# Kernel tuning notes

Hardware: AMD Instinct MI355X
Metric: run time of the kernel (lower is better)

Reference implementation:

```python
import jax, jax.numpy as jnp
import numpy as np

QLEN, MLEN, CMLEN, BSZ, D_MODEL = 1024, 1024, 512, 2, 1024
N_HEAD, D_HEAD, D_INNER = 16, 64, 4096
KLEN = MLEN + CMLEN + QLEN
LN_EPS = 1e-5


def _layer_norm(x, scale, bias):
    mu = jnp.mean(x, axis=-1, keepdims=True)
    var = jnp.var(x, axis=-1, keepdims=True)
    return (x - mu) * jax.lax.rsqrt(var + LN_EPS) * scale + bias


def _rel_shift(x):
    # x: [qlen, klen, bsz, n_head]  (Transformer-XL relative shift)
    q, k, b, n = x.shape
    x = jnp.concatenate([jnp.zeros((q, 1, b, n), x.dtype), x], axis=1)
    x = x.reshape(k + 1, q, b, n)[1:]
    return x.reshape(q, k, b, n)


def setup_inputs() -> dict:
    key = jax.random.key(0)
    ks = jax.random.split(key, 10)
    s = 0.02
    # causal mask: query i (absolute pos MLEN_TOT+i) cannot attend to key j > MLEN_TOT+i
    mlen_tot = KLEN - QLEN
    i = jnp.arange(QLEN)[:, None]
    j = jnp.arange(KLEN)[None, :]
    attn_mask = j > (i + mlen_tot)
    return {
        "input_ids": jax.random.normal(ks[0], (QLEN, BSZ, D_MODEL), jnp.float32),
        "pos_emb": jax.random.normal(ks[1], (KLEN, D_MODEL), jnp.float32),
        "mem": jax.random.normal(ks[2], (MLEN, BSZ, D_MODEL), jnp.float32),
        "c_mem": jax.random.normal(ks[3], (CMLEN, BSZ, D_MODEL), jnp.float32),
        "attn_mask": attn_mask,
        "qkv_w": jax.random.normal(ks[4], (D_MODEL, 3 * N_HEAD * D_HEAD), jnp.float32) * s,
        "r_w": jax.random.normal(ks[5], (D_MODEL, N_HEAD * D_HEAD), jnp.float32) * s,
        "o_w": jax.random.normal(ks[6], (N_HEAD * D_HEAD, D_MODEL), jnp.float32) * s,
        "r_w_bias": jax.random.normal(ks[7], (N_HEAD, D_HEAD), jnp.float32) * s,
        "r_r_bias": jax.random.normal(ks[8], (N_HEAD, D_HEAD), jnp.float32) * s,
        "ln_attn_scale": jnp.ones((D_MODEL,), jnp.float32),
        "ln_attn_bias": jnp.zeros((D_MODEL,), jnp.float32),
        "ff_w1": jax.random.normal(ks[9], (D_MODEL, D_INNER), jnp.float32) * s,
        "ff_b1": jnp.zeros((D_INNER,), jnp.float32),
        "ff_w2": jax.random.normal(jax.random.fold_in(key, 11), (D_INNER, D_MODEL), jnp.float32) * s,
        "ff_b2": jnp.zeros((D_MODEL,), jnp.float32),
        "ln_ff_scale": jnp.ones((D_MODEL,), jnp.float32),
        "ln_ff_bias": jnp.zeros((D_MODEL,), jnp.float32),
    }


def reference(input_ids, pos_emb, mem, c_mem, attn_mask, qkv_w, r_w, o_w,
              r_w_bias, r_r_bias, ln_attn_scale, ln_attn_bias,
              ff_w1, ff_b1, ff_w2, ff_b2, ln_ff_scale, ln_ff_bias):
    qlen, bsz, d_model = input_ids.shape
    n_head, d_head = r_w_bias.shape
    scale = 1.0 / np.sqrt(d_head)

    # _concat_memories + cat with current sequence (seq-first, dim 0)
    mems = jnp.concatenate([mem, c_mem], axis=0)
    cat = jnp.concatenate([mems, input_ids], axis=0)          # [klen, b, d]

    w_heads = cat @ qkv_w                                     # [klen, b, 3*h*dh]
    w_q, w_k, w_v = jnp.split(w_heads, 3, axis=-1)
    w_q = w_q[-qlen:]
    klen = w_k.shape[0]

    w_q = w_q.reshape(qlen, bsz, n_head, d_head)
    w_k = w_k.reshape(klen, bsz, n_head, d_head)
    w_v = w_v.reshape(klen, bsz, n_head, d_head)
    r_k = (pos_emb @ r_w).reshape(klen, n_head, d_head)       # [klen, h, dh]

    AC = jnp.einsum('ibnd,jbnd->ijbn', w_q + r_w_bias, w_k)
    BD = jnp.einsum('ibnd,jnd->ijbn', w_q + r_r_bias, r_k)
    BD = _rel_shift(BD)
    attn_score = (AC + BD) * scale                            # [q, k, b, h]

    attn_score = jnp.where(attn_mask[:, :, None, None], jnp.float32(-1e30), attn_score)
    attn_prob = jax.nn.softmax(attn_score, axis=1)

    attn_vec = jnp.einsum('ijbn,jbnd->ibnd', attn_prob, w_v)
    attn_vec = attn_vec.reshape(qlen, bsz, n_head * d_head)
    attn_out = attn_vec @ o_w

    # post-lnorm residual (pre_lnorm=False)
    attn_res = _layer_norm(input_ids + attn_out, ln_attn_scale, ln_attn_bias)

    # PositionwiseFF (post-lnorm)
    h = jax.nn.relu(attn_res @ ff_w1 + ff_b1) @ ff_w2 + ff_b2
    out = _layer_norm(attn_res + h, ln_ff_scale, ln_ff_bias)
    return out
```

## Files before the change

kernel.cpp:

```cpp
#include <hip/hip_runtime.h>
#include <hip/hip_bf16.h>

#define QLEN 1024
#define KLEN 2560
#define MTOT 1536
#define BSZ 2
#define NH 16
#define DH 64
#define DMODEL 1024
#define DINNER 4096

typedef short bf16x8 __attribute__((ext_vector_type(8)));
typedef float f32x4  __attribute__((ext_vector_type(4)));

__device__ __forceinline__ short f2bf(float f) {
    union { float f; unsigned u; } v; v.f = f;
    unsigned r = v.u + 0x7FFFu + ((v.u >> 16) & 1u);
    return (short)(r >> 16);
}
__device__ __forceinline__ float bf2f(short s) {
    union { unsigned u; float f; } v; v.u = ((unsigned)(unsigned short)s) << 16;
    return v.f;
}
__device__ __forceinline__ unsigned pack2(float a, float b) {
    unsigned pk;
    asm("v_cvt_pk_bf16_f32 %0, %1, %2" : "=v"(pk) : "v"(a), "v"(b));
    return pk;
}

#define GLOAD16(g, l)                                                        \
    __builtin_amdgcn_global_load_lds(                                        \
        (const __attribute__((address_space(1))) unsigned int*)(g),          \
        (__attribute__((address_space(3))) unsigned int*)(l), 16, 0, 0)

__device__ __forceinline__ void tr_body(
    const float* __restrict__ in, short* __restrict__ out,
    int K, int N, int bx, int by, int tid, float (*ts)[65])
{
    const int k0 = by * 64, n0 = bx * 64;
    const int r = tid >> 2, cb = (tid & 3) * 16;
    #pragma unroll
    for (int u = 0; u < 16; u += 4) {
        const float4 v = *(const float4*)(in + (size_t)(k0 + r) * N + n0 + cb + u);
        ts[r][cb + u] = v.x; ts[r][cb + u + 1] = v.y;
        ts[r][cb + u + 2] = v.z; ts[r][cb + u + 3] = v.w;
    }
    __syncthreads();
    #pragma unroll
    for (int p = 0; p < 4; p++) {
        const int wr_ = (tid >> 4) + p * 16;
        const int c   = (tid & 15) * 4;
        uint2 pk;
        pk.x = pack2(ts[c][wr_], ts[c + 1][wr_]);
        pk.y = pack2(ts[c + 2][wr_], ts[c + 3][wr_]);
        *(uint2*)(out + (size_t)(n0 + wr_) * K + k0 + c) = pk;
    }
}

__global__ __launch_bounds__(256) void prep_all(
    const float* __restrict__ mem, const float* __restrict__ cmem,
    const float* __restrict__ inp, short* __restrict__ catb,
    const float* __restrict__ pos, short* __restrict__ posb,
    const float* __restrict__ qkv_w, short* __restrict__ qkv_wt,
    const float* __restrict__ r_w, short* __restrict__ r_wt,
    const float* __restrict__ o_w, short* __restrict__ o_wt,
    const float* __restrict__ ff_w1, short* __restrict__ ff1t,
    const float* __restrict__ ff_w2, short* __restrict__ ff2t)
{
    __shared__ float ts[64][65];
    const int bid = blockIdx.x;
    const int tid = threadIdx.x;
    if (bid < 2560) {
        const int i = bid * 256 + tid;
        const int row = i >> 7, c = (i & 127) * 8;
        const float* src;
        if (row < 2048)      src = mem  + (size_t)row * 1024;
        else if (row < 3072) src = cmem + (size_t)(row - 2048) * 1024;
        else                 src = inp  + (size_t)(row - 3072) * 1024;
        const float4 a = *(const float4*)(src + c);
        const float4 b = *(const float4*)(src + c + 4);
        uint4 o;
        o.x = pack2(a.x, a.y); o.y = pack2(a.z, a.w);
        o.z = pack2(b.x, b.y); o.w = pack2(b.z, b.w);
        *(uint4*)(catb + (size_t)i * 8) = o;
    } else if (bid < 3840) {
        const int i = (bid - 2560) * 256 + tid;
        const float4 a = *(const float4*)(pos + (size_t)i * 8);
        const float4 b = *(const float4*)(pos + (size_t)i * 8 + 4);
        uint4 o;
        o.x = pack2(a.x, a.y); o.y = pack2(a.z, a.w);
        o.z = pack2(b.x, b.y); o.w = pack2(b.z, b.w);
        *(uint4*)(posb + (size_t)i * 8) = o;
    } else if (bid < 4608) {
        const int r = bid - 3840; tr_body(qkv_w, qkv_wt, 1024, 3072, r % 48, r / 48, tid, ts);
    } else if (bid < 4864) {
        const int r = bid - 4608; tr_body(r_w, r_wt, 1024, 1024, r % 16, r / 16, tid, ts);
    } else if (bid < 5120) {
        const int r = bid - 4864; tr_body(o_w, o_wt, 1024, 1024, r % 16, r / 16, tid, ts);
    } else if (bid < 6144) {
        const int r = bid - 5120; tr_body(ff_w1, ff1t, 1024, 4096, r % 64, r / 64, tid, ts);
    } else {
        const int r = bid - 6144; tr_body(ff_w2, ff2t, 4096, 1024, r % 16, r / 16, tid, ts);
    }
}

__global__ __launch_bounds__(256) void vt_conv(
    const short* __restrict__ wh, short* __restrict__ vt)
{
    __shared__ short Ts[64][72];
    const int j0 = blockIdx.x * 64;
    const int bn = blockIdx.y;
    const int b = bn >> 4, n = bn & 15;
    const int tid = threadIdx.x;
    {
        const int key = tid >> 2, c = (tid & 3) * 16;
        const short* p = wh + ((size_t)(j0 + key) * BSZ + b) * 3072 + 2048 + n * 64 + c;
        *(bf16x8*)&Ts[key][c]     = *(const bf16x8*)p;
        *(bf16x8*)&Ts[key][c + 8] = *(const bf16x8*)(p + 8);
    }
    __syncthreads();
    {
        const int d = tid >> 2, kc = (tid & 3) * 16;
        __attribute__((aligned(16))) short tmp[16];
        #pragma unroll
        for (int u = 0; u < 16; u++) tmp[u] = Ts[kc + u][d];
        short* q = vt + ((size_t)(bn * 64) + d) * KLEN + j0 + kc;
        *(uint4*)q       = *(uint4*)tmp;
        *(uint4*)(q + 8) = *((uint4*)tmp + 1);
    }
}

__device__ __forceinline__ void gemm_core(
    const short* __restrict__ A, const short* __restrict__ Bt,
    short* As, short* Bs, int Kfull, int klen, int bm, int bn,
    int tid, f32x4 acc[4][4])
{
    const int w  = tid >> 6;
    const int l  = tid & 63;
    const int lg = l >> 4, lc = l & 15;
    const int wr = w >> 1, wc = w & 1;
    const int srow = 2 * w * 16 + (l >> 2);
    const int scol = (l & 3) * 8;
    const size_t aoff0 = (size_t)(bm + srow) * Kfull + scol;
    const size_t boff0 = (size_t)(bn + srow) * Kfull + scol;
    const size_t rstep = (size_t)16 * Kfull;
    short* lA0 = As + 2 * w * 512;
    short* lA1 = As + (2 * w + 1) * 512;
    short* lB0 = Bs + 2 * w * 512;
    short* lB1 = Bs + (2 * w + 1) * 512;

    for (int k0 = 0; k0 < klen; k0 += 32) {
        GLOAD16(A + aoff0 + k0, lA0);
        GLOAD16(A + aoff0 + rstep + k0, lA1);
        GLOAD16(Bt + boff0 + k0, lB0);
        GLOAD16(Bt + boff0 + rstep + k0, lB1);
        __syncthreads();
        bf16x8 af[4], bfr[4];
        #pragma unroll
        for (int m = 0; m < 4; m++)
            af[m] = *(const bf16x8*)(As + (wr * 64 + m * 16 + lc) * 32 + lg * 8);
        #pragma unroll
        for (int n = 0; n < 4; n++)
            bfr[n] = *(const bf16x8*)(Bs + (wc * 64 + n * 16 + lc) * 32 + lg * 8);
        #pragma unroll
        for (int m = 0; m < 4; m++)
            #pragma unroll
            for (int n = 0; n < 4; n++)
                acc[m][n] = __builtin_amdgcn_mfma_f32_16x16x32_bf16(
                    af[m], bfr[n], acc[m][n], 0, 0, 0);
        __syncthreads();
    }
}

__global__ __launch_bounds__(256) void gemm_g12(
    const short* __restrict__ catb, const short* __restrict__ qkv_wt,
    short* __restrict__ whb,
    const short* __restrict__ posb, const short* __restrict__ r_wt,
    short* __restrict__ rkb)
{
    __shared__ short As[4096], Bs[4096];
    const int tid = threadIdx.x;
    int id = blockIdx.x;
    const short *A, *Bt; short* Cb; int N, bm, bn;
    if (id < 384) {
        A = catb; Bt = qkv_wt; Cb = whb; N = 3072;
        bm = (id >> 4) * 128; bn = (8 + (id & 15)) * 128;
    } else if (id < 768) {
        id -= 384;
        A = catb; Bt = qkv_wt; Cb = whb; N = 3072;
        bm = (24 + id / 24) * 128; bn = (id % 24) * 128;
    } else {
        id -= 768;
        A = posb; Bt = r_wt; Cb = rkb; N = 1024;
        bm = (id / 8) * 128; bn = (id % 8) * 128;
    }

    f32x4 acc[4][4];
    #pragma unroll
    for (int m = 0; m < 4; m++)
        #pragma unroll
        for (int n = 0; n < 4; n++) acc[m][n] = (f32x4){0.f, 0.f, 0.f, 0.f};
    gemm_core(A, Bt, As, Bs, 1024, 1024, bm, bn, tid, acc);

    const int w = tid >> 6, l = tid & 63, lg = l >> 4, lc = l & 15;
    const int wr = w >> 1, wc = w & 1;
    #pragma unroll
    for (int m = 0; m < 4; m++)
        #pragma unroll
        for (int n = 0; n < 4; n++) {
            const int col = bn + wc * 64 + n * 16 + lc;
            #pragma unroll
            for (int r = 0; r < 4; r++) {
                const int row = bm + wr * 64 + m * 16 + lg * 4 + r;
                Cb[(size_t)row * N + col] = f2bf(acc[m][n][r]);
            }
        }
}

__global__ __launch_bounds__(256) void gemm_relu(
    const short* __restrict__ A, const short* __restrict__ Bt,
    const float* __restrict__ bias, short* __restrict__ Cb,
    int N, int K)
{
    __shared__ short As[4096], Bs[4096];
    const int tid = threadIdx.x;
    const int bm = blockIdx.y * 128, bn = blockIdx.x * 128;
    f32x4 acc[4][4];
    #pragma unroll
    for (int m = 0; m < 4; m++)
        #pragma unroll
        for (int n = 0; n < 4; n++) acc[m][n] = (f32x4){0.f, 0.f, 0.f, 0.f};
    gemm_core(A, Bt, As, Bs, K, K, bm, bn, tid, acc);

    const int w = tid >> 6, l = tid & 63, lg = l >> 4, lc = l & 15;
    const int wr = w >> 1, wc = w & 1;
    #pragma unroll
    for (int m = 0; m < 4; m++)
        #pragma unroll
        for (int n = 0; n < 4; n++) {
            const int col = bn + wc * 64 + n * 16 + lc;
            const float bv = bias[col];
            #pragma unroll
            for (int r = 0; r < 4; r++) {
                const int row = bm + wr * 64 + m * 16 + lg * 4 + r;
                Cb[(size_t)row * N + col] = f2bf(fmaxf(acc[m][n][r] + bv, 0.0f));
            }
        }
}

__global__ __launch_bounds__(256) void gemm_split(
    const short* __restrict__ A, const short* __restrict__ Bt,
    float* __restrict__ C0, float* __restrict__ C1,
    int N, int Kfull, int Ksub)
{
    __shared__ short As[4096], Bs[4096];
    const int tid = threadIdx.x;
    const int z = blockIdx.z;
    const int bm = blockIdx.y * 128, bn = blockIdx.x * 128;
    float* C = z ? C1 : C0;
    f32x4 acc[4][4];
    #pragma unroll
    for (int m = 0; m < 4; m++)
        #pragma unroll
        for (int n = 0; n < 4; n++) acc[m][n] = (f32x4){0.f, 0.f, 0.f, 0.f};
    gemm_core(A + z * Ksub, Bt + z * Ksub, As, Bs, Kfull, Ksub, bm, bn, tid, acc);

    const int w = tid >> 6, l = tid & 63, lg = l >> 4, lc = l & 15;
    const int wr = w >> 1, wc = w & 1;
    #pragma unroll
    for (int m = 0; m < 4; m++)
        #pragma unroll
        for (int n = 0; n < 4; n++) {
            const int col = bn + wc * 64 + n * 16 + lc;
            #pragma unroll
            for (int r = 0; r < 4; r++) {
                const int row = bm + wr * 64 + m * 16 + lg * 4 + r;
                C[(size_t)row * N + col] = acc[m][n][r];
            }
        }
}

__global__ __launch_bounds__(512, 2) void attn_mfma(
    const short* __restrict__ wh,
    const short* __restrict__ vt,
    const short* __restrict__ rk,
    const float* __restrict__ rwb,
    const float* __restrict__ rrb,
    short* __restrict__ po,
    float* __restrict__ ml)
{
    __shared__ __align__(16) short Ks[64 * 64];
    __shared__ __align__(16) short Vs[64 * 64];
    __shared__ __align__(16) short Rs[256 * 64];
    __shared__ __align__(16) short Ps[8][16 * 64];

    const int bid = blockIdx.x;
    const int ibp = (bid >> 3) & 7;
    const int z   = (bid >> 6) & 1;
    const int bn  = ((bid & 7) << 2) | (bid >> 7);
    const int i0  = ibp * 128;
    const int b   = bn >> 4, n = bn & 15;
    const int tid = threadIdx.x;
    const int w   = tid >> 6;
    const int l   = tid & 63;
    const int lg  = l >> 4;
    const int lc  = l & 15;
    const int i_base = i0 + 16 * w;

    bf16x8 aqw[2], aqr[2];
    {
        const int i = i_base + lc;
        const short* qp = wh + ((size_t)(MTOT + i) * BSZ + b) * 3072 + n * 64;
        #pragma unroll
        for (int kc2 = 0; kc2 < 2; kc2++) {
            const bf16x8 q8 = *(const bf16x8*)(qp + kc2 * 32 + lg * 8);
            const int d0 = kc2 * 32 + lg * 8;
            #pragma unroll
            for (int e = 0; e < 8; e++) {
                const float qv = bf2f(q8[e]);
                aqw[kc2][e] = f2bf(qv + rwb[n * 64 + d0 + e]);
                aqr[kc2][e] = f2bf(qv + rrb[n * 64 + d0 + e]);
            }
        }
    }

    f32x4 o_acc[4];
    #pragma unroll
    for (int nt = 0; nt < 4; nt++) o_acc[nt] = (f32x4){0.f, 0.f, 0.f, 0.f};
    float mrun[4]  = {0.f, 0.f, 0.f, 0.f};
    float lpart[4] = {0.f, 0.f, 0.f, 0.f};

    const int jend   = i0 + 1664;
    const int jhalf  = i0 / 2 + 832;
    const int jstart = z ? jhalf : 0;
    const int jstop  = z ? jend  : jhalf;

    const int kr = tid >> 3, kc = tid & 7;
    const size_t whK = (size_t)b * 3072 + 1024 + n * 64;
    const size_t vtK = (size_t)(bn * 64) * KLEN;

    {
        const int mbase0 = jstart - i0 + 896;
        #pragma unroll
        for (int u = 0; u < 2; u++) {
            const int m = mbase0 + kr + 64 * u;
            bf16x8 rv = (bf16x8){0, 0, 0, 0, 0, 0, 0, 0};
            if (m < KLEN)
                rv = *(const bf16x8*)(rk + (size_t)m * 1024 + n * 64 + kc * 8);
            const int slot = m & 255;
            *(bf16x8*)(Rs + slot * 64 + ((kc ^ (slot & 7)) * 8)) = rv;
        }
    }
    bf16x8 pk, pv, pr;
    pk = *(const bf16x8*)(wh + (size_t)(jstart + kr) * (BSZ * 3072) + whK + kc * 8);
    pv = *(const bf16x8*)(vt + vtK + (size_t)kr * KLEN + jstart + kc * 8);
    {
        const int m = jstart - i0 + 1024 + kr;
        pr = (m < KLEN)
            ? *(const bf16x8*)(rk + (size_t)m * 1024 + n * 64 + kc * 8)
            : (bf16x8){0, 0, 0, 0, 0, 0, 0, 0};
    }

    for (int j0 = jstart; j0 < jstop; j0 += 64) {
        const int mbase = j0 - i0 + 896;
        __syncthreads();
        *(bf16x8*)(Ks + kr * 64 + ((kc ^ (kr & 7)) * 8)) = pk;
        *(bf16x8*)(Vs + kr * 64 + ((kc ^ (kr & 7)) * 8)) = pv;
        {
            const int slot = (mbase + 128 + kr) & 255;
            *(bf16x8*)(Rs + slot * 64 + ((kc ^ (slot & 7)) * 8)) = pr;
        }
        const int jn = j0 + 64;
        if (jn < jstop) {
            pk = *(const bf16x8*)(wh + (size_t)(jn + kr) * (BSZ * 3072) + whK + kc * 8);
            pv = *(const bf16x8*)(vt + vtK + (size_t)kr * KLEN + jn + kc * 8);
            const int m = jn - i0 + 1024 + kr;
            pr = (m < KLEN)
                ? *(const bf16x8*)(rk + (size_t)m * 1024 + n * 64 + kc * 8)
                : (bf16x8){0, 0, 0, 0, 0, 0, 0, 0};
        }
        __syncthreads();

        __builtin_amdgcn_s_setprio(1);
        f32x4 sfr[4];
        #pragma unroll
        for (int jt = 0; jt < 4; jt++) {
            const int row = 16 * jt + lc;
            const int c0 = (lg ^ (row & 7)) * 8, c1 = ((4 + lg) ^ (row & 7)) * 8;
            const bf16x8 bk0 = *(const bf16x8*)(Ks + row * 64 + c0);
            const bf16x8 bk1 = *(const bf16x8*)(Ks + row * 64 + c1);
            f32x4 acc = (f32x4){0.f, 0.f, 0.f, 0.f};
            acc = __builtin_amdgcn_mfma_f32_16x16x32_bf16(aqw[0], bk0, acc, 0, 0, 0);
            acc = __builtin_amdgcn_mfma_f32_16x16x32_bf16(aqw[1], bk1, acc, 0, 0, 0);
            sfr[jt] = acc;
        }
        f32x4 dr[5];
        #pragma unroll
        for (int mt = 0; mt < 5; mt++) {
            const int slot = (mbase + 16 * mt + lc + 112 - 16 * w) & 255;
            const int c0 = (lg ^ (slot & 7)) * 8, c1 = ((4 + lg) ^ (slot & 7)) * 8;
            const bf16x8 br0 = *(const bf16x8*)(Rs + slot * 64 + c0);
            const bf16x8 br1 = *(const bf16x8*)(Rs + slot * 64 + c1);
            f32x4 acc = (f32x4){0.f, 0.f, 0.f, 0.f};
            acc = __builtin_amdgcn_mfma_f32_16x16x32_bf16(aqr[0], br0, acc, 0, 0, 0);
            acc = __builtin_amdgcn_mfma_f32_16x16x32_bf16(aqr[1], br1, acc, 0, 0, 0);
            dr[mt] = acc;
        }
        __builtin_amdgcn_s_setprio(0);

        #pragma unroll
        for (int r = 0; r < 4; r++) {
            const int q   = 4 * lg + r;
            const int o   = lc + 15 - q;
            const int src = (l & 48) | (o & 15);
            float sv[4];
            float mx = -1e30f;
            #pragma unroll
            for (int jt = 0; jt < 4; jt++) {
                const float v0 = __shfl(dr[jt][r], src);
                const float v1 = __shfl(dr[jt + 1][r], src);
                const float bd = (o < 16) ? v0 : v1;
                float s = (sfr[jt][r] + bd) * 0.125f;
                if (z) {
                    const int j = j0 + 16 * jt + lc;
                    if (j > i_base + q + MTOT) s = -1e30f;
                }
                sv[jt] = s;
                mx = fmaxf(mx, s);
            }
            if (__any(mx - mrun[r] > 8.0f)) {
                #pragma unroll
                for (int msk = 1; msk <= 8; msk <<= 1)
                    mx = fmaxf(mx, __shfl_xor(mx, msk));
                const float mnew = fmaxf(mrun[r], mx);
                const float corr = __expf(mrun[r] - mnew);
                mrun[r] = mnew;
                lpart[r] *= corr;
                #pragma unroll
                for (int nt = 0; nt < 4; nt++) o_acc[nt][r] *= corr;
            }
            float p0 = __expf(sv[0] - mrun[r]);
            float p1 = __expf(sv[1] - mrun[r]);
            float p2 = __expf(sv[2] - mrun[r]);
            float p3 = __expf(sv[3] - mrun[r]);
            lpart[r] += (p0 + p1) + (p2 + p3);
            const unsigned pk01 = pack2(p0, p1);
            const unsigned pk23 = pack2(p2, p3);
            short* pw = Ps[w] + q * 64 + (lc & 7);
            const int qs = q & 7;
            pw[(((0 + (lc >> 3)) ^ qs) * 8)] = (short)(pk01 & 0xffffu);
            pw[(((2 + (lc >> 3)) ^ qs) * 8)] = (short)(pk01 >> 16);
            pw[(((4 + (lc >> 3)) ^ qs) * 8)] = (short)(pk23 & 0xffffu);
            pw[(((6 + (lc >> 3)) ^ qs) * 8)] = (short)(pk23 >> 16);
        }

        asm volatile("s_waitcnt lgkmcnt(0)" ::: "memory");
        __builtin_amdgcn_sched_barrier(0);

        __builtin_amdgcn_s_setprio(1);
        const int pc0 = (lg ^ (lc & 7)) * 8, pc1 = ((4 + lg) ^ (lc & 7)) * 8;
        const bf16x8 pa0 = *(const bf16x8*)(Ps[w] + lc * 64 + pc0);
        const bf16x8 pa1 = *(const bf16x8*)(Ps[w] + lc * 64 + pc1);
        #pragma unroll
        for (int nt = 0; nt < 4; nt++) {
            const int row = 16 * nt + lc;
            const int c0 = (lg ^ (row & 7)) * 8, c1 = ((4 + lg) ^ (row & 7)) * 8;
            const bf16x8 bv0 = *(const bf16x8*)(Vs + row * 64 + c0);
            const bf16x8 bv1 = *(const bf16x8*)(Vs + row * 64 + c1);
            o_acc[nt] = __builtin_amdgcn_mfma_f32_16x16x32_bf16(pa0, bv0, o_acc[nt], 0, 0, 0);
            o_acc[nt] = __builtin_amdgcn_mfma_f32_16x16x32_bf16(pa1, bv1, o_acc[nt], 0, 0, 0);
        }
        __builtin_amdgcn_s_setprio(0);
    }

    const size_t blk = (size_t)z * 256 + ibp * 32 + bn;
    #pragma unroll
    for (int r = 0; r < 4; r++) {
        float lr = lpart[r];
        #pragma unroll
        for (int msk = 1; msk <= 8; msk <<= 1)
            lr += __shfl_xor(lr, msk);
        const int q = 16 * w + 4 * lg + r;
        #pragma unroll
        for (int nt = 0; nt < 4; nt++)
            po[(blk * 128 + q) * 64 + 16 * nt + lc] = f2bf(o_acc[nt][r]);
        if (lc == 0) {
            ml[(blk * 128 + q) * 2 + 0] = mrun[r];
            ml[(blk * 128 + q) * 2 + 1] = lr;
        }
    }
}

__global__ __launch_bounds__(256) void attn_merge(
    const short* __restrict__ po, const float* __restrict__ ml,
    short* __restrict__ av)
{
    const int blk = blockIdx.x;
    const int ib2 = blk >> 5, bn = blk & 31;
    const int b = bn >> 4, n = bn & 15;
    const int tid = threadIdx.x;
    const int q64 = tid >> 2, dc = (tid & 3) * 16;
    const int i = ib2 * 64 + q64;
    const size_t r0 = ((size_t)(i >> 7) * 32 + bn) * 128 + (i & 127);
    const size_t r1 = ((size_t)(256 + (i >> 7) * 32 + bn)) * 128 + (i & 127);
    const float m0 = ml[r0 * 2], l0 = ml[r0 * 2 + 1];
    const float m1 = ml[r1 * 2], l1 = ml[r1 * 2 + 1];
    const float M = fmaxf(m0, m1);
    const float c0 = __expf(m0 - M), c1 = __expf(m1 - M);
    const float invL = 1.0f / (l0 * c0 + l1 * c1);
    const bf16x8 a0 = *(const bf16x8*)(po + r0 * 64 + dc);
    const bf16x8 a1 = *(const bf16x8*)(po + r0 * 64 + dc + 8);
    const bf16x8 b0 = *(const bf16x8*)(po + r1 * 64 + dc);
    const bf16x8 b1 = *(const bf16x8*)(po + r1 * 64 + dc + 8);
    __attribute__((aligned(16))) short ov[16];
    #pragma unroll
    for (int e = 0; e < 8; e++) {
        ov[e]     = f2bf((bf2f(a0[e]) * c0 + bf2f(b0[e]) * c1) * invL);
        ov[e + 8] = f2bf((bf2f(a1[e]) * c0 + bf2f(b1[e]) * c1) * invL);
    }
    short* op = av + ((size_t)i * BSZ + b) * 1024 + n * 64 + dc;
    *(uint4*)op       = *(uint4*)ov;
    *(uint4*)(op + 8) = *((uint4*)ov + 1);
}

template <bool WB, bool HASB>
__global__ __launch_bounds__(256) void ln_fuse(
    const float* __restrict__ p0, const float* __restrict__ p1,
    const float* __restrict__ badd, const float* __restrict__ res,
    const float* __restrict__ scale, const float* __restrict__ bias,
    float* __restrict__ out, short* __restrict__ outb)
{
    const int row = blockIdx.x;
    const int tid = threadIdx.x;
    const size_t base = (size_t)row * 1024 + tid * 4;
    const float4 a = *(const float4*)(p0 + base);
    const float4 b = *(const float4*)(p1 + base);
    const float4 rv = *(const float4*)(res + base);
    float v[4] = {a.x + b.x + rv.x, a.y + b.y + rv.y,
                  a.z + b.z + rv.z, a.w + b.w + rv.w};
    if (HASB) {
        const float4 bb = *(const float4*)(badd + tid * 4);
        v[0] += bb.x; v[1] += bb.y; v[2] += bb.z; v[3] += bb.w;
    }
    float s  = v[0] + v[1] + v[2] + v[3];
    float ss = v[0]*v[0] + v[1]*v[1] + v[2]*v[2] + v[3]*v[3];
    #pragma unroll
    for (int off = 32; off >= 1; off >>= 1) {
        s  += __shfl_down(s, off);
        ss += __shfl_down(ss, off);
    }
    __shared__ float red[8];
    const int lane = tid & 63, wid = tid >> 6;
    if (lane == 0) { red[wid] = s; red[4 + wid] = ss; }
    __syncthreads();
    if (tid == 0) {
        red[0] = red[0] + red[1] + red[2] + red[3];
        red[4] = red[4] + red[5] + red[6] + red[7];
    }
    __syncthreads();
    const float mean = red[0] * (1.0f / 1024.0f);
    const float var  = red[4] * (1.0f / 1024.0f) - mean * mean;
    const float rstd = rsqrtf(var + 1e-5f);
    const float4 sc = *(const float4*)(scale + tid * 4);
    const float4 bi = *(const float4*)(bias + tid * 4);
    float4 o;
    o.x = (v[0] - mean) * rstd * sc.x + bi.x;
    o.y = (v[1] - mean) * rstd * sc.y + bi.y;
    o.z = (v[2] - mean) * rstd * sc.z + bi.z;
    o.w = (v[3] - mean) * rstd * sc.w + bi.w;
    *(float4*)(out + base) = o;
    if (WB) {
        uint2 pk;
        pk.x = pack2(o.x, o.y);
        pk.y = pack2(o.z, o.w);
        *(uint2*)(outb + base) = pk;
    }
}

extern "C" void kernel_launch(void* const* d_in, const int* in_sizes, int n_in,
                              void* d_out, int out_size, void* d_ws, size_t ws_size,
                              hipStream_t stream) {
    const float* input_ids = (const float*)d_in[0];
    const float* pos_emb   = (const float*)d_in[1];
    const float* mem       = (const float*)d_in[2];
    const float* c_mem     = (const float*)d_in[3];
    const float* qkv_w     = (const float*)d_in[5];
    const float* r_w       = (const float*)d_in[6];
    const float* o_w       = (const float*)d_in[7];
    const float* r_w_bias  = (const float*)d_in[8];
    const float* r_r_bias  = (const float*)d_in[9];
    const float* ln_a_s    = (const float*)d_in[10];
    const float* ln_a_b    = (const float*)d_in[11];
    const float* ff_w1     = (const float*)d_in[12];
    const float* ff_b1     = (const float*)d_in[13];
    const float* ff_w2     = (const float*)d_in[14];
    const float* ff_b2     = (const float*)d_in[15];
    const float* ln_f_s    = (const float*)d_in[16];
    const float* ln_f_b    = (const float*)d_in[17];

    char* base = (char*)d_ws;
    short* o_wt   = (short*)(base + 0);
    short* ff1t   = (short*)(base + 2097152);
    short* ff2t   = (short*)(base + 10485760);
    short* whb    = (short*)(base + 18874368);
    short* rkb    = (short*)(base + 50331648);
    short* qkv_wt = (short*)(base + 55574528);
    short* catb   = (short*)(base + 61865984);
    short* posb   = (short*)(base + 72351744);
    short* r_wt   = (short*)(base + 77594624);
    short* vtb    = (short*)(base + 55574528);
    short* po     = (short*)(base + 66060288);
    float* mlb    = (float*)(base + 74448896);
    short* avb    = (short*)(base + 74973184);
    float* hp0    = (float*)(base + 18874368);
    float* hp1    = (float*)(base + 27262976);
    float* ares   = (float*)(base + 35651584);
    short* aresb  = (short*)(base + 44040192);
    short* h1b    = (short*)(base + 48234496);

    const dim3 thr(256);

    prep_all<<<dim3(7168), thr, 0, stream>>>(
        mem, c_mem, input_ids, catb, pos_emb, posb,
        qkv_w, qkv_wt, r_w, r_wt, o_w, o_wt, ff_w1, ff1t, ff_w2, ff2t);
    gemm_g12<<<dim3(928), thr, 0, stream>>>(catb, qkv_wt, whb, posb, r_wt, rkb);
    vt_conv<<<dim3(40, 32), thr, 0, stream>>>(whb, vtb);
    attn_mfma<<<dim3(512), dim3(512), 0, stream>>>(
        whb, vtb, rkb, r_w_bias, r_r_bias, po, mlb);
    attn_merge<<<dim3(512), thr, 0, stream>>>(po, mlb, avb);
    gemm_split<<<dim3(8, 16, 2), thr, 0, stream>>>(
        avb, o_wt, hp0, hp1, 1024, 1024, 512);
    ln_fuse<true, false><<<dim3(2048), thr, 0, stream>>>(
        hp0, hp1, nullptr, input_ids, ln_a_s, ln_a_b, ares, aresb);
    gemm_relu<<<dim3(32, 16), thr, 0, stream>>>(aresb, ff1t, ff_b1, h1b, 4096, 1024);
    gemm_split<<<dim3(8, 16, 2), thr, 0, stream>>>(
        h1b, ff2t, hp0, hp1, 1024, 4096, 2048);
    ln_fuse<false, true><<<dim3(2048), thr, 0, stream>>>(
        hp0, hp1, ff_b2, ares, ln_f_s, ln_f_b, (float*)d_out, nullptr);
}
```

Before: 274.3 us.

## Double-buffer K/V tiles in attention and XCD-swizzle GEMM block mapping

The attention kernel now keeps two LDS buffers for the K and V tiles and prefetches two tiles ahead. This lets it drop the second __syncthreads per iteration, and the R ring buffer is pre-filled one tile further ahead. Separately, all GEMM kernels switch to a 1D grid whose block index is swizzled across the 8 XCDs, so neighbouring tiles share an L2. The double buffering adds LDS use, which may limit occupancy at 2 blocks of 512 threads. The R-slot indexing across the 256-row ring must also stay correct, since one barrier was removed.

Result: no change. 273.9 us (-0.1%).

```diff
diff --git a/kernel.cpp b/kernel.cpp
--- a/kernel.cpp
+++ b/kernel.cpp
@@ -180,7 +180,8 @@
 {
     __shared__ short As[4096], Bs[4096];
     const int tid = threadIdx.x;
-    int id = blockIdx.x;
+    const int id0 = blockIdx.x;
+    int id = (id0 & 7) * 116 + (id0 >> 3);
     const short *A, *Bt; short* Cb; int N, bm, bn;
     if (id < 384) {
         A = catb; Bt = qkv_wt; Cb = whb; N = 3072;
@@ -224,7 +225,11 @@
 {
     __shared__ short As[4096], Bs[4096];
     const int tid = threadIdx.x;
-    const int bm = blockIdx.y * 128, bn = blockIdx.x * 128;
+    const int nbx = N >> 7;
+    const int lid = blockIdx.x;
+    const int nwg8 = gridDim.x >> 3;
+    const int swz = (lid & 7) * nwg8 + (lid >> 3);
+    const int bn = (swz % nbx) * 128, bm = (swz / nbx) * 128;
     f32x4 acc[4][4];
     #pragma unroll
     for (int m = 0; m < 4; m++)
@@ -255,8 +260,14 @@
 {
     __shared__ short As[4096], Bs[4096];
     const int tid = threadIdx.x;
-    const int z = blockIdx.z;
-    const int bm = blockIdx.y * 128, bn = blockIdx.x * 128;
+    const int nbx = N >> 7;
+    const int lid = blockIdx.x;
+    const int nwg8 = gridDim.x >> 3;
+    const int swz = (lid & 7) * nwg8 + (lid >> 3);
+    const int bn = (swz % nbx) * 128;
+    const int rest = swz / nbx;
+    const int bm = (rest & 15) * 128;
+    const int z = rest >> 4;
     float* C = z ? C1 : C0;
     f32x4 acc[4][4];
     #pragma unroll
@@ -289,8 +300,8 @@
     short* __restrict__ po,
     float* __restrict__ ml)
 {
-    __shared__ __align__(16) short Ks[64 * 64];
-    __shared__ __align__(16) short Vs[64 * 64];
+    __shared__ __align__(16) short Ks[2][64 * 64];
+    __shared__ __align__(16) short Vs[2][64 * 64];
     __shared__ __align__(16) short Rs[256 * 64];
     __shared__ __align__(16) short Ps[8][16 * 64];
 
@@ -338,48 +349,56 @@
     const int kr = tid >> 3, kc = tid & 7;
     const size_t whK = (size_t)b * 3072 + 1024 + n * 64;
     const size_t vtK = (size_t)(bn * 64) * KLEN;
-
+    const int mbase0 = jstart - i0 + 896;
+
+    #pragma unroll
+    for (int u = 0; u < 3; u++) {
+        const int m = mbase0 + kr + 64 * u;
+        bf16x8 rv = (bf16x8){0, 0, 0, 0, 0, 0, 0, 0};
+        if (m < KLEN)
+            rv = *(const bf16x8*)(rk + (size_t)m * 1024 + n * 64 + kc * 8);
+        const int slot = m & 255;
+        *(bf16x8*)(Rs + slot * 64 + ((kc ^ (slot & 7)) * 8)) = rv;
+    }
     {
-        const int mbase0 = jstart - i0 + 896;
-        #pragma unroll
-        for (int u = 0; u < 2; u++) {
-            const int m = mbase0 + kr + 64 * u;
-            bf16x8 rv = (bf16x8){0, 0, 0, 0, 0, 0, 0, 0};
-            if (m < KLEN)
-                rv = *(const bf16x8*)(rk + (size_t)m * 1024 + n * 64 + kc * 8);
-            const int slot = m & 255;
-            *(bf16x8*)(Rs + slot * 64 + ((kc ^ (slot & 7)) * 8)) = rv;
-        }
-    }
-    bf16x8 pk, pv, pr;
-    pk = *(const bf16x8*)(wh + (size_t)(jstart + kr) * (BSZ * 3072) + whK + kc * 8);
-    pv = *(const bf16x8*)(vt + vtK + (size_t)kr * KLEN + jstart + kc * 8);
+        const bf16x8 k0 = *(const bf16x8*)(wh + (size_t)(jstart + kr) * (BSZ * 3072) + whK + kc * 8);
+        const bf16x8 v0 = *(const bf16x8*)(vt + vtK + (size_t)kr * KLEN + jstart + kc * 8);
+        *(bf16x8*)(Ks[0] + kr * 64 + ((kc ^ (kr & 7)) * 8)) = k0;
+        *(bf16x8*)(Vs[0] + kr * 64 + ((kc ^ (kr & 7)) * 8)) = v0;
+    }
+    bf16x8 pk = (bf16x8){0,0,0,0,0,0,0,0}, pv = pk, pr;
     {
-        const int m = jstart - i0 + 1024 + kr;
-        pr = (m < KLEN)
-            ? *(const bf16x8*)(rk + (size_t)m * 1024 + n * 64 + kc * 8)
-            : (bf16x8){0, 0, 0, 0, 0, 0, 0, 0};
-    }
-
+        const int jn = jstart + 64;
+        if (jn < jstop) {
+            pk = *(const bf16x8*)(wh + (size_t)(jn + kr) * (BSZ * 3072) + whK + kc * 8);
+            pv = *(const bf16x8*)(vt + vtK + (size_t)kr * KLEN + jn + kc * 8);
+        }
+        const int m = mbase0 + 192 + kr;
+        pr = (m < KLEN) ? *(const bf16x8*)(rk + (size_t)m * 1024 + n * 64 + kc * 8)
+                        : (bf16x8){0, 0, 0, 0, 0, 0, 0, 0};
+    }
+
+    int cur = 0;
     for (int j0 = jstart; j0 < jstop; j0 += 64) {
         const int mbase = j0 - i0 + 896;
         __syncthreads();
-        *(bf16x8*)(Ks + kr * 64 + ((kc ^ (kr & 7)) * 8)) = pk;
-        *(bf16x8*)(Vs + kr * 64 + ((kc ^ (kr & 7)) * 8)) = pv;
+        *(bf16x8*)(Ks[cur ^ 1] + kr * 64 + ((kc ^ (kr & 7)) * 8)) = pk;
+        *(bf16x8*)(Vs[cur ^ 1] + kr * 64 + ((kc ^ (kr & 7)) * 8)) = pv;
         {
-            const int slot = (mbase + 128 + kr) & 255;
+            const int mw = mbase + 192 + kr;
+            const int slot = mw & 255;
             *(bf16x8*)(Rs + slot * 64 + ((kc ^ (slot & 7)) * 8)) = pr;
         }
-        const int jn = j0 + 64;
-        if (jn < jstop) {
-            pk = *(const bf16x8*)(wh + (size_t)(jn + kr) * (BSZ * 3072) + whK + kc * 8);
-            pv = *(const bf16x8*)(vt + vtK + (size_t)kr * KLEN + jn + kc * 8);
-            const int m = jn - i0 + 1024 + kr;
-            pr = (m < KLEN)
-                ? *(const bf16x8*)(rk + (size_t)m * 1024 + n * 64 + kc * 8)
-                : (bf16x8){0, 0, 0, 0, 0, 0, 0, 0};
-        }
-        __syncthreads();
+        {
+            const int jn = j0 + 128;
+            if (jn < jstop) {
+                pk = *(const bf16x8*)(wh + (size_t)(jn + kr) * (BSZ * 3072) + whK + kc * 8);
+                pv = *(const bf16x8*)(vt + vtK + (size_t)kr * KLEN + jn + kc * 8);
+            }
+            const int m = mbase + 256 + kr;
+            pr = (m < KLEN) ? *(const bf16x8*)(rk + (size_t)m * 1024 + n * 64 + kc * 8)
+                            : (bf16x8){0, 0, 0, 0, 0, 0, 0, 0};
+        }
 
         __builtin_amdgcn_s_setprio(1);
         f32x4 sfr[4];
@@ -387,8 +406,8 @@
         for (int jt = 0; jt < 4; jt++) {
             const int row = 16 * jt + lc;
             const int c0 = (lg ^ (row & 7)) * 8, c1 = ((4 + lg) ^ (row & 7)) * 8;
-            const bf16x8 bk0 = *(const bf16x8*)(Ks + row * 64 + c0);
-            const bf16x8 bk1 = *(const bf16x8*)(Ks + row * 64 + c1);
+            const bf16x8 bk0 = *(const bf16x8*)(Ks[cur] + row * 64 + c0);
+            const bf16x8 bk1 = *(const bf16x8*)(Ks[cur] + row * 64 + c1);
             f32x4 acc = (f32x4){0.f, 0.f, 0.f, 0.f};
             acc = __builtin_amdgcn_mfma_f32_16x16x32_bf16(aqw[0], bk0, acc, 0, 0, 0);
             acc = __builtin_amdgcn_mfma_f32_16x16x32_bf16(aqw[1], bk1, acc, 0, 0, 0);
@@ -465,12 +484,13 @@
         for (int nt = 0; nt < 4; nt++) {
             const int row = 16 * nt + lc;
             const int c0 = (lg ^ (row & 7)) * 8, c1 = ((4 + lg) ^ (row & 7)) * 8;
-            const bf16x8 bv0 = *(const bf16x8*)(Vs + row * 64 + c0);
-            const bf16x8 bv1 = *(const bf16x8*)(Vs + row * 64 + c1);
+            const bf16x8 bv0 = *(const bf16x8*)(Vs[cur] + row * 64 + c0);
+            const bf16x8 bv1 = *(const bf16x8*)(Vs[cur] + row * 64 + c1);
             o_acc[nt] = __builtin_amdgcn_mfma_f32_16x16x32_bf16(pa0, bv0, o_acc[nt], 0, 0, 0);
             o_acc[nt] = __builtin_amdgcn_mfma_f32_16x16x32_bf16(pa1, bv1, o_acc[nt], 0, 0, 0);
         }
         __builtin_amdgcn_s_setprio(0);
+        cur ^= 1;
     }
 
     const size_t blk = (size_t)z * 256 + ibp * 32 + bn;
@@ -628,12 +648,12 @@
     attn_mfma<<<dim3(512), dim3(512), 0, stream>>>(
         whb, vtb, rkb, r_w_bias, r_r_bias, po, mlb);
     attn_merge<<<dim3(512), thr, 0, stream>>>(po, mlb, avb);
-    gemm_split<<<dim3(8, 16, 2), thr, 0, stream>>>(
+    gemm_split<<<dim3(256), thr, 0, stream>>>(
         avb, o_wt, hp0, hp1, 1024, 1024, 512);
     ln_fuse<true, false><<<dim3(2048), thr, 0, stream>>>(
         hp0, hp1, nullptr, input_ids, ln_a_s, ln_a_b, ares, aresb);
-    gemm_relu<<<dim3(32, 16), thr, 0, stream>>>(aresb, ff1t, ff_b1, h1b, 4096, 1024);
-    gemm_split<<<dim3(8, 16, 2), thr, 0, stream>>>(
+    gemm_relu<<<dim3(512), thr, 0, stream>>>(aresb, ff1t, ff_b1, h1b, 4096, 1024);
+    gemm_split<<<dim3(256), thr, 0, stream>>>(
         h1b, ff2t, hp0, hp1, 1024, 4096, 2048);
     ln_fuse<false, true><<<dim3(2048), thr, 0, stream>>>(
         hp0, hp1, ff_b2, ares, ln_f_s, ln_f_b, (float*)d_out, nullptr);
```
